# Performance work log

Hardware: AMD Instinct MI355X
Metric: run time of the kernel (lower is better)

## Reference

```python
import jax, jax.numpy as jnp
import numpy as np

B, T, H = 16, 512, 1024
L, D = 8192, 256

def setup_inputs() -> dict:
    key = jax.random.key(0)
    k1, k2, k3, k4, k5 = jax.random.split(key, 5)
    X = jax.random.normal(k1, (B, T, H), dtype=jnp.float32)
    attention_mask = jnp.ones((B, T), dtype=jnp.int32)
    queries = jax.random.normal(k2, (L, D), dtype=jnp.float32) * 0.02
    Wk = jax.random.normal(k3, (D, H), dtype=jnp.float32) * (1.0 / np.sqrt(H))
    Wv = jax.random.normal(k4, (D, H), dtype=jnp.float32) * (1.0 / np.sqrt(H))
    out_weight = jax.random.normal(k5, (L, D), dtype=jnp.float32) * 0.02
    out_bias = jnp.zeros((L,), dtype=jnp.float32)
    return {"X": X, "attention_mask": attention_mask, "queries": queries,
            "Wk": Wk, "Wv": Wv, "out_weight": out_weight, "out_bias": out_bias}

def reference(X, attention_mask, queries, Wk, Wv, out_weight, out_bias):
    # K, V: [B, T, D] (nn.Linear with weight [D, H], no bias)
    K = jnp.einsum('bth,dh->btd', X, Wk)
    V = jnp.einsum('bth,dh->btd', X, Wv)
    scale = 1.0 / jnp.sqrt(jnp.asarray(K.shape[-1], dtype=K.dtype))
    # attention logits: [B, L, T]
    attn_logits = jnp.einsum('ld,btd->blt', queries, K) * scale
    neg = jnp.finfo(attn_logits.dtype).min
    attn_logits = jnp.where(attention_mask[:, None, :] == 0, neg, attn_logits)
    attn = jax.nn.softmax(attn_logits, axis=-1)
    # per-label context: [B, L, D]
    ctx = jnp.einsum('blt,btd->bld', attn, V)
    # fused per-label output projection: [B, L]
    logits = jnp.einsum('bld,ld->bl', ctx, out_weight) + out_bias[None, :]
    return logits
```

## Files before the change

### kernel.cpp

```cpp
#include <hip/hip_runtime.h>
#include <hip/hip_bf16.h>


typedef __bf16 bf16x8 __attribute__((ext_vector_type(8)));
typedef float f32x4 __attribute__((ext_vector_type(4)));

__device__ __forceinline__ unsigned short f2bf(float f) {
    unsigned int u = __builtin_bit_cast(unsigned int, f);
    unsigned int lsb = (u >> 16) & 1u;
    u += 0x7fffu + lsb;
    return (unsigned short)(u >> 16);
}

__device__ __forceinline__ void gld_lds16(const void* g, void* l) {
    __builtin_amdgcn_global_load_lds((__attribute__((address_space(1))) void*)g,
                                     (__attribute__((address_space(3))) void*)l,
                                     16, 0, 0);
}

__global__ __launch_bounds__(256) void cvt_all(const float* __restrict__ X,
                                               const float* __restrict__ Q,
                                               const float* __restrict__ Wo,
                                               const float* __restrict__ Wk,
                                               const float* __restrict__ Wv,
                                               unsigned short* __restrict__ dst) {
    int base = blockIdx.x * 1024 + threadIdx.x;
#pragma unroll
    for (int r = 0; r < 4; ++r) {
        int idx = base + r * 256;
        const float* src;
        int off;
        float s = 1.0f;
        if (idx < 2097152)      { src = X;  off = idx; }
        else if (idx < 2621440) { src = Q;  off = idx - 2097152; s = 0.09016844006f; }
        else if (idx < 3145728) { src = Wo; off = idx - 2621440; }
        else if (idx < 3211264) { src = Wk; off = idx - 3145728; }
        else                    { src = Wv; off = idx - 3211264; }
        float4 v = ((const float4*)src)[off];
        ushort4 o;
        o.x = f2bf(v.x * s); o.y = f2bf(v.y * s);
        o.z = f2bf(v.z * s); o.w = f2bf(v.w * s);
        ((ushort4*)dst)[idx] = o;
    }
}

__global__ __launch_bounds__(256) void kv_gemm(const unsigned short* __restrict__ Xb,
                                               const unsigned short* __restrict__ Wb,
                                               unsigned short* __restrict__ Kb,
                                               unsigned short* __restrict__ Vb) {
    __shared__ unsigned short Xs[2][128 * 64];
    __shared__ unsigned short Ws[2][128 * 64];
    const int bid = blockIdx.x;
    const int nt = bid & 3, mt = bid >> 2;
    const int m0 = mt * 128, n0 = nt * 128;
    const int tid = threadIdx.x;
    const int lane = tid & 63, w = tid >> 6;
    const int q = lane >> 4, ln = lane & 15;
    const int wm = (w & 1) * 64, wn = (w >> 1) * 64;
    const int lrow = lane >> 3;
    const int gsw  = (lane & 7) ^ lrow;

    f32x4 acc[4][4];
#pragma unroll
    for (int mi = 0; mi < 4; ++mi)
#pragma unroll
        for (int ni = 0; ni < 4; ++ni) acc[mi][ni] = f32x4{0.f, 0.f, 0.f, 0.f};

    auto stage = [&](int hc) {
        const int p = hc & 1;
        const int h0 = hc * 64;
#pragma unroll
        for (int j = 0; j < 4; ++j) {
            int slot = w * 4 + j;
            int r = slot * 8 + lrow;
            gld_lds16(Xb + (size_t)(m0 + r) * 1024 + h0 + gsw * 8,
                      &Xs[p][slot * 512]);
            gld_lds16(Wb + (size_t)(n0 + r) * 1024 + h0 + gsw * 8,
                      &Ws[p][slot * 512]);
        }
    };
    stage(0);

#pragma unroll 1
    for (int hc = 0; hc < 16; ++hc) {
        asm volatile("s_waitcnt vmcnt(0)" ::: "memory");
        __syncthreads();
        if (hc < 15) stage(hc + 1);
        const int p = hc & 1;
#pragma unroll
        for (int ks = 0; ks < 64; ks += 32) {
            bf16x8 a[4], b[4];
#pragma unroll
            for (int mi = 0; mi < 4; ++mi) {
                int r = wm + mi * 16 + ln;
                int g = ((ks >> 3) + q) ^ (r & 7);
                a[mi] = *(const bf16x8*)(&Xs[p][r * 64 + g * 8]);
            }
#pragma unroll
            for (int ni = 0; ni < 4; ++ni) {
                int r = wn + ni * 16 + ln;
                int g = ((ks >> 3) + q) ^ (r & 7);
                b[ni] = *(const bf16x8*)(&Ws[p][r * 64 + g * 8]);
            }
#pragma unroll
            for (int mi = 0; mi < 4; ++mi)
#pragma unroll
                for (int ni = 0; ni < 4; ++ni)
                    acc[mi][ni] = __builtin_amdgcn_mfma_f32_16x16x32_bf16(
                        a[mi], b[ni], acc[mi][ni], 0, 0, 0);
        }
        __syncthreads();
    }
    {
        unsigned short* dst = (n0 < 256) ? Kb : Vb;
        const int d0 = (n0 & 255) + wn;
#pragma unroll
        for (int mi = 0; mi < 4; ++mi)
#pragma unroll
            for (int ni = 0; ni < 4; ++ni) {
                int d = d0 + ni * 16 + ln;
#pragma unroll
                for (int r = 0; r < 4; ++r) {
                    int m = m0 + wm + mi * 16 + q * 4 + r;
                    dst[m * 256 + d] = f2bf(acc[mi][ni][r]);
                }
            }
    }
}

__global__ __launch_bounds__(256, 2) void attn_fused(const unsigned short* __restrict__ Qb,
                                                     const unsigned short* __restrict__ Wob,
                                                     const unsigned short* __restrict__ Kb,
                                                     const unsigned short* __restrict__ Vb,
                                                     const int* __restrict__ mask,
                                                     const float* __restrict__ bias,
                                                     float* __restrict__ out) {
    __shared__ unsigned short Ks[2][8192];
    __shared__ unsigned short Vs[2][8192];
    const int bid = blockIdx.x;
    const int bb = bid >> 6;
    const int l0 = (bid & 63) * 128;
    const int tid = threadIdx.x;
    const int lane = tid & 63, w = tid >> 6;
    const int q = lane >> 4, ln = lane & 15;
    const int hi = lane >> 5, lo = lane & 31;

    auto stage = [&](int c) {
        const int p = c & 1;
        const int rbase = bb * 512 + c * 32;
#pragma unroll
        for (int j = 0; j < 8; ++j) {
            int gid = w * 8 + j;
            int g = gid & 15;
            const unsigned short* srcb = (gid < 16) ? Kb : Vb;
            unsigned short* dstb = (gid < 16) ? &Ks[p][0] : &Vs[p][0];
            int tl = 2 * g + hi;
            gld_lds16(srcb + (size_t)(rbase + tl) * 256 + ((lo ^ tl) << 3),
                      dstb + g * 512);
        }
    };
    stage(0);

    unsigned mbits = 0;
    {
        const int* mrow = mask + bb * 512;
#pragma unroll
        for (int j = 0; j < 32; ++j)
            mbits |= (mrow[j * 16 + ln] != 0 ? 1u : 0u) << j;
    }

    bf16x8 aQ[2][8], aW[2][8];
#pragma unroll
    for (int mi = 0; mi < 2; ++mi) {
        const int row = (l0 + w * 32 + mi * 16 + ln) * 256;
#pragma unroll
        for (int kk = 0; kk < 8; ++kk) {
            aQ[mi][kk] = *(const bf16x8*)(&Qb[row + kk * 32 + q * 8]);
            aW[mi][kk] = *(const bf16x8*)(&Wob[row + kk * 32 + q * 8]);
        }
    }

    float num[2][4], den[2][4];
#pragma unroll
    for (int mi = 0; mi < 2; ++mi)
#pragma unroll
        for (int r = 0; r < 4; ++r) { num[mi][r] = 0.f; den[mi][r] = 0.f; }

#pragma unroll 1
    for (int c = 0; c < 16; ++c) {
        asm volatile("s_waitcnt vmcnt(0)" ::: "memory");
        __syncthreads();
        if (c < 15) stage(c + 1);
        const int p = c & 1;

        f32x4 Sa[2][2], Pa[2][2];
#pragma unroll
        for (int mi = 0; mi < 2; ++mi)
#pragma unroll
            for (int ni = 0; ni < 2; ++ni) {
                Sa[mi][ni] = f32x4{0.f, 0.f, 0.f, 0.f};
                Pa[mi][ni] = f32x4{0.f, 0.f, 0.f, 0.f};
            }

#pragma unroll
        for (int kk = 0; kk < 8; ++kk) {
            bf16x8 bK[2], bV[2];
#pragma unroll
            for (int ni = 0; ni < 2; ++ni) {
                const int t = ni * 16 + ln;
                const int off = t * 256 + (((kk * 4 + q) ^ t) << 3);
                bK[ni] = *(const bf16x8*)(&Ks[p][off]);
                bV[ni] = *(const bf16x8*)(&Vs[p][off]);
            }
#pragma unroll
            for (int mi = 0; mi < 2; ++mi)
#pragma unroll
                for (int ni = 0; ni < 2; ++ni) {
                    Sa[mi][ni] = __builtin_amdgcn_mfma_f32_16x16x32_bf16(
                        aQ[mi][kk], bK[ni], Sa[mi][ni], 0, 0, 0);
                    Pa[mi][ni] = __builtin_amdgcn_mfma_f32_16x16x32_bf16(
                        aW[mi][kk], bV[ni], Pa[mi][ni], 0, 0, 0);
                }
        }
#pragma unroll
        for (int ni = 0; ni < 2; ++ni) {
            bool ok = (mbits >> (c * 2 + ni)) & 1u;
#pragma unroll
            for (int mi = 0; mi < 2; ++mi)
#pragma unroll
                for (int r = 0; r < 4; ++r) {
                    float e = ok ? __builtin_amdgcn_exp2f(Sa[mi][ni][r]) : 0.0f;
                    den[mi][r] += e;
                    num[mi][r] += e * Pa[mi][ni][r];
                }
        }
    }

#pragma unroll
    for (int mi = 0; mi < 2; ++mi)
#pragma unroll
        for (int r = 0; r < 4; ++r) {
            float n_ = num[mi][r], d_ = den[mi][r];
#pragma unroll
            for (int o = 1; o < 16; o <<= 1) {
                n_ += __shfl_xor(n_, o);
                d_ += __shfl_xor(d_, o);
            }
            if (ln == 0) {
                int l = l0 + w * 32 + mi * 16 + q * 4 + r;
                out[bb * 8192 + l] = n_ / d_ + bias[l];
            }
        }
}

extern "C" void kernel_launch(void* const* d_in, const int* in_sizes, int n_in,
                              void* d_out, int out_size, void* d_ws, size_t ws_size,
                              hipStream_t stream) {
    const float* X    = (const float*)d_in[0];
    const int*   mask = (const int*)d_in[1];
    const float* Q    = (const float*)d_in[2];
    const float* Wk   = (const float*)d_in[3];
    const float* Wv   = (const float*)d_in[4];
    const float* Wo   = (const float*)d_in[5];
    const float* bias = (const float*)d_in[6];
    float* out = (float*)d_out;

    unsigned short* Xb   = (unsigned short*)d_ws;
    unsigned short* Qb   = Xb + 8388608ull;
    unsigned short* Wob  = Qb + 2097152ull;
    unsigned short* Wkvb = Wob + 2097152ull;
    unsigned short* Kb   = Wkvb + 524288ull;
    unsigned short* Vb   = Kb + 2097152ull;

    cvt_all<<<dim3(3200), 256, 0, stream>>>(X, Q, Wo, Wk, Wv, Xb);
    kv_gemm<<<dim3(256), 256, 0, stream>>>(Xb, Wkvb, Kb, Vb);
    attn_fused<<<dim3(1024), 256, 0, stream>>>(Qb, Wob, Kb, Vb, mask, bias, out);
}
```

Before: 192.2 us.

## Switch attention kernel to 32x32x16 MFMA tiles with one tile per wave

Each wave now computes its 32 labels x 32 tokens score and projection tiles with a single 32x32x16 bf16 MFMA chain instead of four 16x16x32 MFMAs per k-step. The operand fragments, the per-token mask bits, the LDS read pattern and the final 32-lane shuffle reduction are remapped to the 32x32 output layout. The aim is to halve the LDS B-operand reads per MFMA and cut instruction count, using larger MFMA tiles. In exchange it adds more shuffle steps at the end and changes the accumulator register layout, which may affect register pressure.

```diff
diff --git a/kernel.cpp b/kernel.cpp
--- a/kernel.cpp
+++ b/kernel.cpp
@@ -4,6 +4,7 @@
 
 typedef __bf16 bf16x8 __attribute__((ext_vector_type(8)));
 typedef float f32x4 __attribute__((ext_vector_type(4)));
+typedef float f32x16 __attribute__((ext_vector_type(16)));
 
 __device__ __forceinline__ unsigned short f2bf(float f) {
     unsigned int u = __builtin_bit_cast(unsigned int, f);
@@ -142,8 +143,8 @@
     const int l0 = (bid & 63) * 128;
     const int tid = threadIdx.x;
     const int lane = tid & 63, w = tid >> 6;
-    const int q = lane >> 4, ln = lane & 15;
-    const int hi = lane >> 5, lo = lane & 31;
+    const int t32 = lane & 31;
+    const int hi = lane >> 5;
 
     auto stage = [&](int c) {
         const int p = c & 1;
@@ -155,7 +156,7 @@
             const unsigned short* srcb = (gid < 16) ? Kb : Vb;
             unsigned short* dstb = (gid < 16) ? &Ks[p][0] : &Vs[p][0];
             int tl = 2 * g + hi;
-            gld_lds16(srcb + (size_t)(rbase + tl) * 256 + ((lo ^ tl) << 3),
+            gld_lds16(srcb + (size_t)(rbase + tl) * 256 + ((t32 ^ tl) << 3),
                       dstb + g * 512);
         }
     };
@@ -165,26 +166,23 @@
     {
         const int* mrow = mask + bb * 512;
 #pragma unroll
-        for (int j = 0; j < 32; ++j)
-            mbits |= (mrow[j * 16 + ln] != 0 ? 1u : 0u) << j;
-    }
-
-    bf16x8 aQ[2][8], aW[2][8];
-#pragma unroll
-    for (int mi = 0; mi < 2; ++mi) {
-        const int row = (l0 + w * 32 + mi * 16 + ln) * 256;
-#pragma unroll
-        for (int kk = 0; kk < 8; ++kk) {
-            aQ[mi][kk] = *(const bf16x8*)(&Qb[row + kk * 32 + q * 8]);
-            aW[mi][kk] = *(const bf16x8*)(&Wob[row + kk * 32 + q * 8]);
-        }
-    }
-
-    float num[2][4], den[2][4];
-#pragma unroll
-    for (int mi = 0; mi < 2; ++mi)
-#pragma unroll
-        for (int r = 0; r < 4; ++r) { num[mi][r] = 0.f; den[mi][r] = 0.f; }
+        for (int j = 0; j < 16; ++j)
+            mbits |= (mrow[j * 32 + t32] != 0 ? 1u : 0u) << j;
+    }
+
+    bf16x8 aQ[16], aW[16];
+    {
+        const int arow = (l0 + w * 32 + t32) * 256;
+#pragma unroll
+        for (int ks = 0; ks < 16; ++ks) {
+            aQ[ks] = *(const bf16x8*)(&Qb[arow + ks * 16 + hi * 8]);
+            aW[ks] = *(const bf16x8*)(&Wob[arow + ks * 16 + hi * 8]);
+        }
+    }
+
+    float num[16], den[16];
+#pragma unroll
+    for (int r = 0; r < 16; ++r) { num[r] = 0.f; den[r] = 0.f; }
 
 #pragma unroll 1
     for (int c = 0; c < 16; ++c) {
@@ -193,64 +191,43 @@
         if (c < 15) stage(c + 1);
         const int p = c & 1;
 
-        f32x4 Sa[2][2], Pa[2][2];
-#pragma unroll
-        for (int mi = 0; mi < 2; ++mi)
-#pragma unroll
-            for (int ni = 0; ni < 2; ++ni) {
-                Sa[mi][ni] = f32x4{0.f, 0.f, 0.f, 0.f};
-                Pa[mi][ni] = f32x4{0.f, 0.f, 0.f, 0.f};
-            }
-
-#pragma unroll
-        for (int kk = 0; kk < 8; ++kk) {
-            bf16x8 bK[2], bV[2];
-#pragma unroll
-            for (int ni = 0; ni < 2; ++ni) {
-                const int t = ni * 16 + ln;
-                const int off = t * 256 + (((kk * 4 + q) ^ t) << 3);
-                bK[ni] = *(const bf16x8*)(&Ks[p][off]);
-                bV[ni] = *(const bf16x8*)(&Vs[p][off]);
-            }
-#pragma unroll
-            for (int mi = 0; mi < 2; ++mi)
-#pragma unroll
-                for (int ni = 0; ni < 2; ++ni) {
-                    Sa[mi][ni] = __builtin_amdgcn_mfma_f32_16x16x32_bf16(
-                        aQ[mi][kk], bK[ni], Sa[mi][ni], 0, 0, 0);
-                    Pa[mi][ni] = __builtin_amdgcn_mfma_f32_16x16x32_bf16(
-                        aW[mi][kk], bV[ni], Pa[mi][ni], 0, 0, 0);
-                }
-        }
-#pragma unroll
-        for (int ni = 0; ni < 2; ++ni) {
-            bool ok = (mbits >> (c * 2 + ni)) & 1u;
-#pragma unroll
-            for (int mi = 0; mi < 2; ++mi)
-#pragma unroll
-                for (int r = 0; r < 4; ++r) {
-                    float e = ok ? __builtin_amdgcn_exp2f(Sa[mi][ni][r]) : 0.0f;
-                    den[mi][r] += e;
-                    num[mi][r] += e * Pa[mi][ni][r];
-                }
-        }
-    }
-
-#pragma unroll
-    for (int mi = 0; mi < 2; ++mi)
-#pragma unroll
-        for (int r = 0; r < 4; ++r) {
-            float n_ = num[mi][r], d_ = den[mi][r];
-#pragma unroll
-            for (int o = 1; o < 16; o <<= 1) {
-                n_ += __shfl_xor(n_, o);
-                d_ += __shfl_xor(d_, o);
-            }
-            if (ln == 0) {
-                int l = l0 + w * 32 + mi * 16 + q * 4 + r;
-                out[bb * 8192 + l] = n_ / d_ + bias[l];
-            }
-        }
+        f32x16 Sa, Pa;
+#pragma unroll
+        for (int r = 0; r < 16; ++r) { Sa[r] = 0.f; Pa[r] = 0.f; }
+
+#pragma unroll
+        for (int ks = 0; ks < 16; ++ks) {
+            const int gd = ks * 2 + hi;
+            const int off = t32 * 256 + ((gd ^ t32) << 3);
+            bf16x8 bK = *(const bf16x8*)(&Ks[p][off]);
+            bf16x8 bV = *(const bf16x8*)(&Vs[p][off]);
+            Sa = __builtin_amdgcn_mfma_f32_32x32x16_bf16(aQ[ks], bK, Sa, 0, 0, 0);
+            Pa = __builtin_amdgcn_mfma_f32_32x32x16_bf16(aW[ks], bV, Pa, 0, 0, 0);
+        }
+        {
+            bool ok = (mbits >> c) & 1u;
+#pragma unroll
+            for (int r = 0; r < 16; ++r) {
+                float e = ok ? __builtin_amdgcn_exp2f(Sa[r]) : 0.0f;
+                den[r] += e;
+                num[r] += e * Pa[r];
+            }
+        }
+    }
+
+#pragma unroll
+    for (int r = 0; r < 16; ++r) {
+        float n_ = num[r], d_ = den[r];
+#pragma unroll
+        for (int o = 1; o < 32; o <<= 1) {
+            n_ += __shfl_xor(n_, o);
+            d_ += __shfl_xor(d_, o);
+        }
+        if (t32 == 0) {
+            int l = l0 + w * 32 + (r & 3) + 8 * (r >> 2) + 4 * hi;
+            out[bb * 8192 + l] = n_ / d_ + bias[l];
+        }
+    }
 }
 
 extern "C" void kernel_launch(void* const* d_in, const int* in_sizes, int n_in,
```

After: 198.5 us. 1.03x slower.
